# Optimization experiments

Measured on AMD Instinct MI355X. Metric: run time of the kernel, lower is better.

The kernel has to match this reference:

```python
import jax, jax.numpy as jnp
import numpy as np

B, N, M, D, H, K, V = 2, 2048, 2048, 1024, 16, 64, 64
MAX_WAVELENGTH = 10000
SCALE_FACTOR = 1.0


def rope(x, positions, max_wavelength, scale_factor):
    # x: [b, s, h, k]; positions: [b, s] int
    head_dim = x.shape[-1]
    fraction = 2.0 * jnp.arange(head_dim // 2, dtype=x.dtype) / head_dim
    timescale = jnp.asarray(max_wavelength, x.dtype) ** fraction            # [k/2]
    # scaled positions -> phase per (b, s, 1 head bcast, k/2)
    phase = (positions.astype(x.dtype) / scale_factor)[:, :, None, None] / timescale  # [b,s,1,k/2]
    sin, cos = jnp.sin(phase), jnp.cos(phase)
    x1, x2 = jnp.split(x, 2, axis=-1)
    return jnp.concatenate([x1 * cos - x2 * sin, x2 * cos + x1 * sin], axis=-1)


def setup_inputs() -> dict:
    key = jax.random.key(0)
    ks = jax.random.split(key, 8)
    scale = 1.0 / np.sqrt(D)  # keep logits numerically sane with random params
    inp = {
        "query": jax.random.normal(ks[0], (B, N, D), jnp.float32),
        "q_positions": jnp.broadcast_to(jnp.arange(N, dtype=jnp.int32), (B, N)),
        "key": jax.random.normal(ks[1], (B, M, D), jnp.float32),
        "k_positions": jnp.broadcast_to(jnp.arange(M, dtype=jnp.int32), (B, M)),
        "value": jax.random.normal(ks[2], (B, M, D), jnp.float32),
        "mask": jnp.ones((1, 1, N, M), dtype=bool),
        "P_q": jax.random.normal(ks[3], (H, D, K), jnp.float32) * scale,
        "P_k": jax.random.normal(ks[4], (H, D, K), jnp.float32) * scale,
        "P_v": jax.random.normal(ks[5], (H, D, V), jnp.float32) * scale,
        "P_o": jax.random.normal(ks[6], (H, D, V), jnp.float32) * scale,
    }
    return inp


def reference(query, q_positions, key, k_positions, value, mask, P_q, P_k, P_v, P_o):
    q = jnp.einsum('bnd,hdk->bnhk', query, P_q)
    k = jnp.einsum('bmd,hdk->bmhk', key, P_k)
    v = jnp.einsum('bmd,hdv->bmhv', value, P_v)
    q = rope(q, q_positions, MAX_WAVELENGTH, SCALE_FACTOR)
    k = rope(k, k_positions, MAX_WAVELENGTH, SCALE_FACTOR)
    logits = jnp.einsum('bnhk,bmhk->bhnm', q, k)
    if mask is not None:
        logits = jnp.where(mask, logits, -jnp.inf)
    weights = jax.nn.softmax(logits, axis=-1)
    o = jnp.einsum('bhnm,bmhv->bnhv', weights, v)
    return jnp.einsum('bnhv,hdv->bnd', o, P_o)
```

## Files before the change

kernel.cpp:

```cpp
#include <hip/hip_runtime.h>
#include <hip/hip_bf16.h>
#include <math.h>

#define B_ 2
#define N_ 2048
#define M_ 2048
#define D_ 1024
#define H_ 16


typedef _Float16 f16;
typedef f16  f16x2 __attribute__((ext_vector_type(2)));
typedef f16  f16x4 __attribute__((ext_vector_type(4)));
typedef f16  f16x8 __attribute__((ext_vector_type(8)));
typedef float f32x4  __attribute__((ext_vector_type(4)));
typedef float f32x16 __attribute__((ext_vector_type(16)));

#define MFMA16(a, b, c) __builtin_amdgcn_mfma_f32_16x16x32_f16((a), (b), (c), 0, 0, 0)
#define MFMA32(a, b, c) __builtin_amdgcn_mfma_f32_32x32x16_f16((a), (b), (c), 0, 0, 0)
#define LDST 72
#define EXP2(x) __builtin_amdgcn_exp2f(x)

static __device__ __forceinline__ unsigned int pk2(float a, float b) {
  auto h = __builtin_amdgcn_cvt_pkrtz(a, b);
  return __builtin_bit_cast(unsigned int, h);
}
static __device__ __forceinline__ float max3f(float a, float b, float c) {
  return fmaxf(fmaxf(a, b), c);
}

__global__ __launch_bounds__(256) void prep_all(
    const float* __restrict__ Pq, const float* __restrict__ Pk,
    const float* __restrict__ Pv, const float* __restrict__ Po,
    const int* __restrict__ qpos, const int* __restrict__ kpos,
    f16* __restrict__ Ptq, f16* __restrict__ Ptk, f16* __restrict__ Ptv,
    f16* __restrict__ Wo, float2* __restrict__ tabq, float2* __restrict__ tabk)
{
  __shared__ float Ts[64][65];
  const int z = blockIdx.y, x = blockIdx.x, tid = threadIdx.x;
  if (z < 3) {
    if (x >= 256) return;
    const float* P = (z == 0) ? Pq : (z == 1) ? Pk : Pv;
    f16* Pt = (z == 0) ? Ptq : (z == 1) ? Ptk : Ptv;
    const int d0 = (x & 15) * 64, h = x >> 4;
    #pragma unroll
    for (int it = 0; it < 4; ++it) {
      int fi = tid + 256 * it;
      int dr = fi >> 4, c4 = (fi & 15) << 2;
      float4 v = *(const float4*)(P + ((size_t)h * D_ + d0 + dr) * 64 + c4);
      Ts[dr][c4+0] = v.x; Ts[dr][c4+1] = v.y; Ts[dr][c4+2] = v.z; Ts[dr][c4+3] = v.w;
    }
    __syncthreads();
    const int c = tid >> 2, dp = (tid & 3) * 16;
    f16x8 w0, w1;
    #pragma unroll
    for (int i = 0; i < 8; ++i) { w0[i] = (f16)Ts[dp + i][c]; w1[i] = (f16)Ts[dp + 8 + i][c]; }
    f16* dst = Pt + ((size_t)h * 64 + c) * D_ + d0 + dp;
    *(f16x8*)dst = w0;
    *(f16x8*)(dst + 8) = w1;
  } else if (z == 3) {
    int e = (x * 256 + tid) * 4;
    if (e >= H_ * D_ * 64) return;
    int h = e >> 16, d = (e >> 6) & 1023, v = e & 63;
    float4 xx = *(const float4*)(Po + e);
    f16x4 w = {(f16)xx.x, (f16)xx.y, (f16)xx.z, (f16)xx.w};
    *(f16x4*)&Wo[(size_t)d * 1024 + h * 64 + v] = w;
  } else {
    if (x >= 512) return;
    int idx = x * 256 + tid;
    int r = idx >> 5, c = idx & 31;
    const int* pos = (z == 4) ? qpos : kpos;
    float2* tab = (z == 4) ? tabq : tabk;
    float fpos = (float)pos[r];
    float inv_ts = exp2f(-(float)c * 0.4152410118609203f);
    float ph = fpos * inv_ts, sn, cs;
    sincosf(ph, &sn, &cs);
    tab[idx] = make_float2(cs, sn);
  }
}

__global__ __launch_bounds__(256) void gemm_fused(
    const float* __restrict__ Aq, const float* __restrict__ Ak,
    const float* __restrict__ Av,
    const f16* __restrict__ Bq, const f16* __restrict__ Bk,
    const f16* __restrict__ Bv,
    const float2* __restrict__ tabq, const float2* __restrict__ tabk,
    f16* __restrict__ dq, f16* __restrict__ dk, f16* __restrict__ dv)
{
  __shared__ f16 As[128 * LDST];
  __shared__ f16 Bs[128 * LDST];
  const int tid = threadIdx.x, lane = tid & 63, wave = tid >> 6;
  const int quad = lane >> 4, l16 = lane & 15;
  const int lb = blockIdx.x + 8 * (int)blockIdx.y;
  const int xcd = lb & 7, t = lb >> 3;
  const int col0 = (t & 7) * 128;
  const int row0 = (xcd * 4 + (t >> 3)) * 128;
  const int op = blockIdx.z;
  const int wr = (wave >> 1) * 64, wc = (wave & 1) * 64;

  const float* A  = (op == 0) ? Aq : (op == 1) ? Ak : Av;
  const f16*  Bt  = (op == 0) ? Bq : (op == 1) ? Bk : Bv;

  f32x4 acc[4][4] = {};
  float4 apre[8];
  f16x8  bpre[4];

  #pragma unroll
  for (int it = 0; it < 8; ++it) {
    int fi = tid + 256 * it;
    int row = fi >> 4, c4 = (fi & 15) << 2;
    apre[it] = *(const float4*)(A + (size_t)(row0 + row) * 1024 + c4);
  }
  #pragma unroll
  for (int it = 0; it < 4; ++it) {
    int fi = tid + 256 * it;
    int row = fi >> 3, c8 = (fi & 7) * 8;
    bpre[it] = *(const f16x8*)(Bt + (size_t)(col0 + row) * 1024 + c8);
  }

  for (int k0 = 0; k0 < 1024; k0 += 64) {
    __syncthreads();
    #pragma unroll
    for (int it = 0; it < 8; ++it) {
      int fi = tid + 256 * it;
      int row = fi >> 4, c4 = (fi & 15) << 2;
      f16x4 hv = {(f16)apre[it].x, (f16)apre[it].y, (f16)apre[it].z, (f16)apre[it].w};
      *(f16x4*)&As[row * LDST + c4] = hv;
    }
    #pragma unroll
    for (int it = 0; it < 4; ++it) {
      int fi = tid + 256 * it;
      int row = fi >> 3, c8 = (fi & 7) * 8;
      *(f16x8*)&Bs[row * LDST + c8] = bpre[it];
    }
    __syncthreads();
    if (k0 + 64 < 1024) {
      #pragma unroll
      for (int it = 0; it < 8; ++it) {
        int fi = tid + 256 * it;
        int row = fi >> 4, c4 = (fi & 15) << 2;
        apre[it] = *(const float4*)(A + (size_t)(row0 + row) * 1024 + k0 + 64 + c4);
      }
      #pragma unroll
      for (int it = 0; it < 4; ++it) {
        int fi = tid + 256 * it;
        int row = fi >> 3, c8 = (fi & 7) * 8;
        bpre[it] = *(const f16x8*)(Bt + (size_t)(col0 + row) * 1024 + k0 + 64 + c8);
      }
    }
    #pragma unroll
    for (int ks = 0; ks < 2; ++ks) {
      f16x8 af[4], bf[4];
      #pragma unroll
      for (int i = 0; i < 4; ++i)
        af[i] = *(const f16x8*)&As[(wr + i * 16 + l16) * LDST + ks * 32 + quad * 8];
      #pragma unroll
      for (int j = 0; j < 4; ++j)
        bf[j] = *(const f16x8*)&Bs[(wc + j * 16 + l16) * LDST + ks * 32 + quad * 8];
      #pragma unroll
      for (int i = 0; i < 4; ++i)
        #pragma unroll
        for (int j = 0; j < 4; ++j)
          acc[i][j] = MFMA16(af[i], bf[j], acc[i][j]);
    }
  }

  if (op == 2) {
    #pragma unroll
    for (int i = 0; i < 4; ++i) {
      int r = row0 + wr + i * 16 + quad * 4;
      int b = r >> 11, s = r & 2047;
      #pragma unroll
      for (int j = 0; j < 4; ++j) {
        int col = col0 + wc + j * 16 + l16;
        int h = col >> 6, v = col & 63;
        f16x4 w = {(f16)acc[i][j][0], (f16)acc[i][j][1],
                   (f16)acc[i][j][2], (f16)acc[i][j][3]};
        *(f16x4*)&dv[((size_t)(b * H_ + h) * 64 + v) * 2048 + s] = w;
      }
    }
  } else {
    const float2* tab = (op == 0) ? tabq : tabk;
    f16* oq = (op == 0) ? dq : dk;
    #pragma unroll
    for (int i = 0; i < 4; ++i) {
      #pragma unroll
      for (int reg = 0; reg < 4; ++reg) {
        int r = row0 + wr + i * 16 + quad * 4 + reg;
        int b = r >> 11, s = r & 2047;
        #pragma unroll
        for (int j = 0; j < 2; ++j) {
          int col = col0 + wc + j * 16 + l16;
          int h = col >> 6, c = col & 63;
          float2 cs = tab[r * 32 + c];
          float x1 = acc[i][j][reg], x2 = acc[i][j + 2][reg];
          size_t base = ((size_t)(b * H_ + h) * 2048 + s) * 64;
          oq[base + c]      = (f16)(x1 * cs.x - x2 * cs.y);
          oq[base + c + 32] = (f16)(x2 * cs.x + x1 * cs.y);
        }
      }
    }
  }
}

__global__ __launch_bounds__(512, 4) void flash7b(
    const f16* __restrict__ q, const f16* __restrict__ k,
    const f16* __restrict__ vt, f16* __restrict__ o)
{
  __shared__ __align__(16) char smem[4 * 64 * LDST * sizeof(f16)];

  const int tid = threadIdx.x, lane = tid & 63, wave = tid >> 6;
  const int g = wave >> 2, w4 = wave & 3;
  const int L = lane >> 5, nl = lane & 31;
  const int lin = blockIdx.x + 16 * (blockIdx.y + 16 * (int)blockIdx.z);
  const int xcd = lin & 7, t = lin >> 3;
  const int hb = xcd * 4 + (t >> 4);
  const int n0 = (t & 15) * 128;
  const int h = hb & 15, b = hb >> 4;

  f16* Ks  = (f16*)smem + (size_t)g * (64 * LDST);
  f16* Vts = (f16*)smem + (size_t)(2 + g) * (64 * LDST);

  const f16* qb = q  + (size_t)(b * H_ + h) * N_ * 64;
  const f16* kb = k  + (size_t)(b * H_ + h) * M_ * 64 + (size_t)g * 1024 * 64;
  const f16* vb = vt + (size_t)(b * H_ + h) * 64 * M_ + g * 1024;

  f16x8 qf[4];
  #pragma unroll
  for (int gg = 0; gg < 4; ++gg)
    qf[gg] = *(const f16x8*)(qb + (size_t)(n0 + w4 * 32 + nl) * 64 + gg * 16 + L * 8);

  f32x16 acc[2] = {};
  float mst = -INFINITY;
  float lst = 0.f;
  const float L2E = 1.4426950408889634f;

  const int gtid = tid & 255;
  const int srow = gtid >> 2, soff = (gtid & 3) * 16;

  f16x8 kp0 = *(const f16x8*)(kb + (size_t)srow * 64 + soff);
  f16x8 kp1 = *(const f16x8*)(kb + (size_t)srow * 64 + soff + 8);
  f16x8 vp0 = *(const f16x8*)(vb + (size_t)srow * M_ + soff);
  f16x8 vp1 = *(const f16x8*)(vb + (size_t)srow * M_ + soff + 8);

  for (int m0 = 0; m0 < 1024; m0 += 64) {
    __syncthreads();
    *(f16x8*)&Ks[srow * LDST + soff]      = kp0;
    *(f16x8*)&Ks[srow * LDST + soff + 8]  = kp1;
    *(f16x8*)&Vts[srow * LDST + soff]     = vp0;
    *(f16x8*)&Vts[srow * LDST + soff + 8] = vp1;
    __syncthreads();
    if (m0 + 64 < 1024) {
      kp0 = *(const f16x8*)(kb + (size_t)(m0 + 64 + srow) * 64 + soff);
      kp1 = *(const f16x8*)(kb + (size_t)(m0 + 64 + srow) * 64 + soff + 8);
      vp0 = *(const f16x8*)(vb + (size_t)srow * M_ + m0 + 64 + soff);
      vp1 = *(const f16x8*)(vb + (size_t)srow * M_ + m0 + 64 + soff + 8);
    }

    f32x16 s[2] = {};
    __builtin_amdgcn_s_setprio(1);
    #pragma unroll
    for (int u = 0; u < 2; ++u)
      #pragma unroll
      for (int gg = 0; gg < 4; ++gg) {
        f16x8 af = *(const f16x8*)&Ks[(u * 32 + nl) * LDST + gg * 16 + L * 8];
        s[u] = MFMA32(af, qf[gg], s[u]);
      }
    __builtin_amdgcn_s_setprio(0);

    float a11[11];
    #pragma unroll
    for (int i = 0; i < 10; ++i) {
      int j = 3 * i;
      float x0 = (j < 16) ? s[0][j] : s[1][j - 16];
      float x1 = (j + 1 < 16) ? s[0][j + 1] : s[1][j - 15];
      float x2 = (j + 2 < 16) ? s[0][j + 2] : s[1][j - 14];
      a11[i] = max3f(x0, x1, x2);
    }
    a11[10] = fmaxf(s[1][14], s[1][15]);
    float b4_0 = max3f(a11[0], a11[1], a11[2]);
    float b4_1 = max3f(a11[3], a11[4], a11[5]);
    float b4_2 = max3f(a11[6], a11[7], a11[8]);
    float b4_3 = fmaxf(a11[9], a11[10]);
    float mx = fmaxf(fmaxf(b4_0, b4_1), fmaxf(b4_2, b4_3));
    mx = fmaxf(mx, __shfl_xor(mx, 32));
    float mx2 = mx * L2E;
    float m_new = fmaxf(mst, mx2);

    if (!__all(mx2 - mst <= 8.0f)) {
      float alpha = EXP2(mst - m_new);
      #pragma unroll
      for (int u = 0; u < 2; ++u)
        #pragma unroll
        for (int r = 0; r < 16; ++r) acc[u][r] *= alpha;
      lst *= alpha;
      mst = m_new;
    }

    #pragma unroll
    for (int u = 0; u < 2; ++u)
      #pragma unroll
      for (int r = 0; r < 16; ++r)
        s[u][r] = EXP2(s[u][r] * L2E - mst);

    unsigned int qw[2][4][2];
    #pragma unroll
    for (int u = 0; u < 2; ++u)
      #pragma unroll
      for (int rq = 0; rq < 4; ++rq) {
        qw[u][rq][0] = pk2(s[u][rq * 4 + 0], s[u][rq * 4 + 1]);
        qw[u][rq][1] = pk2(s[u][rq * 4 + 2], s[u][rq * 4 + 3]);
      }

#if __has_builtin(__builtin_amdgcn_fdot2)
    {
      const f16x2 one2 = {(f16)1.0f, (f16)1.0f};
      float sum = 0.f;
      #pragma unroll
      for (int u = 0; u < 2; ++u)
        #pragma unroll
        for (int rq = 0; rq < 4; ++rq)
          #pragma unroll
          for (int w = 0; w < 2; ++w)
            sum = __builtin_amdgcn_fdot2(
                __builtin_bit_cast(f16x2, qw[u][rq][w]), one2, sum, false);
      sum += __shfl_xor(sum, 32);
      lst += sum;
    }
#else
    {
      float ts[16];
      #pragma unroll
      for (int r = 0; r < 16; ++r) ts[r] = s[0][r] + s[1][r];
      #pragma unroll
      for (int st = 8; st >= 1; st >>= 1)
        #pragma unroll
        for (int r = 0; r < st; ++r) ts[r] += ts[r + st];
      float sum = ts[0];
      sum += __shfl_xor(sum, 32);
      lst += sum;
    }
#endif

    union PBu { unsigned int w[4]; f16x8 v; } pb[4];
    #pragma unroll
    for (int u = 0; u < 2; ++u)
      #pragma unroll
      for (int gg = 0; gg < 2; ++gg)
        #pragma unroll
        for (int w = 0; w < 2; ++w) {
          unsigned int a = qw[u][2 * gg][w], bb = qw[u][2 * gg + 1][w];
          asm volatile("v_permlane32_swap_b32 %0, %1" : "+v"(a), "+v"(bb));
          pb[2 * u + gg].w[w]     = a;
          pb[2 * u + gg].w[2 + w] = bb;
        }

    __builtin_amdgcn_s_setprio(1);
    #pragma unroll
    for (int u = 0; u < 2; ++u)
      #pragma unroll
      for (int gg = 0; gg < 4; ++gg) {
        f16x8 vf = *(const f16x8*)&Vts[(u * 32 + nl) * LDST + gg * 16 + L * 8];
        acc[u] = MFMA32(vf, pb[gg].v, acc[u]);
      }
    __builtin_amdgcn_s_setprio(0);
  }

  float* mrg = (float*)smem;
  const int mb = (w4 * 64 + lane) * 34;
  __syncthreads();
  if (g == 1) {
    #pragma unroll
    for (int r = 0; r < 16; ++r) { mrg[mb + r] = acc[0][r]; mrg[mb + 16 + r] = acc[1][r]; }
    mrg[mb + 32] = mst;
    mrg[mb + 33] = lst;
  }
  __syncthreads();
  if (g == 0) {
    float m1 = mrg[mb + 32], l1 = mrg[mb + 33];
    float Mm = fmaxf(mst, m1);
    float a0 = EXP2(mst - Mm), a1 = EXP2(m1 - Mm);
    float invl = 1.0f / (a0 * lst + a1 * l1);
    f16* ob = o + ((size_t)(b * N_ + n0 + w4 * 32 + nl) * 1024) + h * 64;
    #pragma unroll
    for (int u = 0; u < 2; ++u)
      #pragma unroll
      for (int rq = 0; rq < 4; ++rq) {
        f16x4 w;
        #pragma unroll
        for (int j = 0; j < 4; ++j)
          w[j] = (f16)((a0 * acc[u][rq * 4 + j] + a1 * mrg[mb + u * 16 + rq * 4 + j]) * invl);
        *(f16x4*)&ob[u * 32 + 8 * rq + 4 * L] = w;
      }
  }
}

__global__ __launch_bounds__(256) void gemm_out(
    const f16* __restrict__ A, const f16* __restrict__ Bt,
    float* __restrict__ out)
{
  __shared__ f16 As[128 * LDST];
  __shared__ f16 Bs[64 * LDST];
  const int tid = threadIdx.x, lane = tid & 63, wave = tid >> 6;
  const int quad = lane >> 4, l16 = lane & 15;
  const int lb = blockIdx.x + 16 * (int)blockIdx.y;
  const int xcd = lb & 7, t = lb >> 3;
  const int col0 = (t & 15) * 64;
  const int row0 = (xcd * 4 + (t >> 4)) * 128;
  const int wr = (wave >> 1) * 64, wc = (wave & 1) * 32;

  f32x4 acc[4][2] = {};
  f16x8 apre[4], bpre[2];

  #pragma unroll
  for (int it = 0; it < 4; ++it) {
    int fi = tid + 256 * it;
    int row = fi >> 3, c8 = (fi & 7) * 8;
    apre[it] = *(const f16x8*)(A + (size_t)(row0 + row) * 1024 + c8);
  }
  #pragma unroll
  for (int it = 0; it < 2; ++it) {
    int fi = tid + 256 * it;
    int row = fi >> 3, c8 = (fi & 7) * 8;
    bpre[it] = *(const f16x8*)(Bt + (size_t)(col0 + row) * 1024 + c8);
  }

  for (int k0 = 0; k0 < 1024; k0 += 64) {
    __syncthreads();
    #pragma unroll
    for (int it = 0; it < 4; ++it) {
      int fi = tid + 256 * it;
      int row = fi >> 3, c8 = (fi & 7) * 8;
      *(f16x8*)&As[row * LDST + c8] = apre[it];
    }
    #pragma unroll
    for (int it = 0; it < 2; ++it) {
      int fi = tid + 256 * it;
      int row = fi >> 3, c8 = (fi & 7) * 8;
      *(f16x8*)&Bs[row * LDST + c8] = bpre[it];
    }
    __syncthreads();
    if (k0 + 64 < 1024) {
      #pragma unroll
      for (int it = 0; it < 4; ++it) {
        int fi = tid + 256 * it;
        int row = fi >> 3, c8 = (fi & 7) * 8;
        apre[it] = *(const f16x8*)(A + (size_t)(row0 + row) * 1024 + k0 + 64 + c8);
      }
      #pragma unroll
      for (int it = 0; it < 2; ++it) {
        int fi = tid + 256 * it;
        int row = fi >> 3, c8 = (fi & 7) * 8;
        bpre[it] = *(const f16x8*)(Bt + (size_t)(col0 + row) * 1024 + k0 + 64 + c8);
      }
    }
    #pragma unroll
    for (int ks = 0; ks < 2; ++ks) {
      f16x8 af[4], bf[2];
      #pragma unroll
      for (int i = 0; i < 4; ++i)
        af[i] = *(const f16x8*)&As[(wr + i * 16 + l16) * LDST + ks * 32 + quad * 8];
      #pragma unroll
      for (int j = 0; j < 2; ++j)
        bf[j] = *(const f16x8*)&Bs[(wc + j * 16 + l16) * LDST + ks * 32 + quad * 8];
      #pragma unroll
      for (int i = 0; i < 4; ++i)
        #pragma unroll
        for (int j = 0; j < 2; ++j)
          acc[i][j] = MFMA16(af[i], bf[j], acc[i][j]);
    }
  }

  #pragma unroll
  for (int i = 0; i < 4; ++i)
    #pragma unroll
    for (int j = 0; j < 2; ++j)
      #pragma unroll
      for (int reg = 0; reg < 4; ++reg)
        out[(size_t)(row0 + wr + i * 16 + quad * 4 + reg) * 1024 +
            col0 + wc + j * 16 + l16] = acc[i][j][reg];
}

extern "C" void kernel_launch(void* const* d_in, const int* in_sizes, int n_in,
                              void* d_out, int out_size, void* d_ws, size_t ws_size,
                              hipStream_t stream) {
  (void)in_sizes; (void)n_in; (void)out_size; (void)ws_size;
  const float* query = (const float*)d_in[0];
  const int*   qpos  = (const int*)d_in[1];
  const float* key   = (const float*)d_in[2];
  const int*   kpos  = (const int*)d_in[3];
  const float* value = (const float*)d_in[4];
  const float* Pq = (const float*)d_in[6];
  const float* Pk = (const float*)d_in[7];
  const float* Pv = (const float*)d_in[8];
  const float* Po = (const float*)d_in[9];
  float* out = (float*)d_out;

  const size_t pm = (size_t)1024 * 1024;
  const size_t em = (size_t)B_ * H_ * 2048 * 64;
  f16* Ptq = (f16*)d_ws;
  f16* Ptk = Ptq + pm;
  f16* Ptv = Ptk + pm;
  f16* Wo  = Ptv + pm;
  f16* q_ws  = Wo + pm;
  f16* k_ws  = q_ws + em;
  f16* vt_ws = k_ws + em;
  f16* o_ws  = vt_ws + em;
  float2* tabq = (float2*)(o_ws + em);
  float2* tabk = tabq + (size_t)4096 * 32;

  dim3 blk(256);
  prep_all<<<dim3(1024, 6), blk, 0, stream>>>(
      Pq, Pk, Pv, Po, qpos, kpos, Ptq, Ptk, Ptv, Wo, tabq, tabk);

  gemm_fused<<<dim3(8, 32, 3), blk, 0, stream>>>(
      query, key, value, Ptq, Ptk, Ptv, tabq, tabk, q_ws, k_ws, vt_ws);

  flash7b<<<dim3(N_ / 128, H_, B_), dim3(512), 0, stream>>>(q_ws, k_ws, vt_ws, o_ws);

  gemm_out<<<dim3(16, 32), blk, 0, stream>>>(o_ws, Wo, out);
}
```

Before: 232.9 us.

## Pre-convert activations to fp16 and stage GEMM tiles via direct global-to-LDS loads

Adds a conversion pass in the prep kernel that casts query/key/value from fp32 to fp16 in workspace, so the projection GEMM reads half-width activations. Both the projection GEMM and the output GEMM now fill shared memory with global_load_lds (16-byte direct-to-LDS) instead of register prefetch plus ds_write. The padded LDS stride is dropped to fit the direct-load layout. In exchange, the register-level double-buffer overlap is gone, the extra conversion pass costs a full fp32 read plus fp16 write of the activations, and the unpadded layout may cause LDS bank conflicts on fragment reads.

```diff
diff --git a/kernel.cpp b/kernel.cpp
--- a/kernel.cpp
+++ b/kernel.cpp
@@ -21,6 +21,11 @@
 #define LDST 72
 #define EXP2(x) __builtin_amdgcn_exp2f(x)
 
+#define GLOAD_LDS(g, l)                                             \
+  __builtin_amdgcn_global_load_lds(                                 \
+      (const __attribute__((address_space(1))) void*)(g),           \
+      (__attribute__((address_space(3))) void*)(l), 16, 0, 0)
+
 static __device__ __forceinline__ unsigned int pk2(float a, float b) {
   auto h = __builtin_amdgcn_cvt_pkrtz(a, b);
   return __builtin_bit_cast(unsigned int, h);
@@ -33,8 +38,11 @@
     const float* __restrict__ Pq, const float* __restrict__ Pk,
     const float* __restrict__ Pv, const float* __restrict__ Po,
     const int* __restrict__ qpos, const int* __restrict__ kpos,
+    const float* __restrict__ Aq, const float* __restrict__ Ak,
+    const float* __restrict__ Av,
     f16* __restrict__ Ptq, f16* __restrict__ Ptk, f16* __restrict__ Ptv,
-    f16* __restrict__ Wo, float2* __restrict__ tabq, float2* __restrict__ tabk)
+    f16* __restrict__ Wo, float2* __restrict__ tabq, float2* __restrict__ tabk,
+    f16* __restrict__ A16q, f16* __restrict__ A16k, f16* __restrict__ A16v)
 {
   __shared__ float Ts[64][65];
   const int z = blockIdx.y, x = blockIdx.x, tid = threadIdx.x;
@@ -65,7 +73,7 @@
     float4 xx = *(const float4*)(Po + e);
     f16x4 w = {(f16)xx.x, (f16)xx.y, (f16)xx.z, (f16)xx.w};
     *(f16x4*)&Wo[(size_t)d * 1024 + h * 64 + v] = w;
-  } else {
+  } else if (z < 6) {
     if (x >= 512) return;
     int idx = x * 256 + tid;
     int r = idx >> 5, c = idx & 31;
@@ -76,19 +84,31 @@
     float ph = fpos * inv_ts, sn, cs;
     sincosf(ph, &sn, &cs);
     tab[idx] = make_float2(cs, sn);
+  } else {
+    const float* s = (z == 6) ? Aq : (z == 7) ? Ak : Av;
+    f16* d = (z == 6) ? A16q : (z == 7) ? A16k : A16v;
+    size_t e = ((size_t)x * 256 + tid) * 16;
+    #pragma unroll
+    for (int half = 0; half < 2; ++half) {
+      float4 v0 = *(const float4*)(s + e + half * 8);
+      float4 v1 = *(const float4*)(s + e + half * 8 + 4);
+      f16x8 w = {(f16)v0.x, (f16)v0.y, (f16)v0.z, (f16)v0.w,
+                 (f16)v1.x, (f16)v1.y, (f16)v1.z, (f16)v1.w};
+      *(f16x8*)(d + e + half * 8) = w;
+    }
   }
 }
 
 __global__ __launch_bounds__(256) void gemm_fused(
-    const float* __restrict__ Aq, const float* __restrict__ Ak,
-    const float* __restrict__ Av,
+    const f16* __restrict__ Aq, const f16* __restrict__ Ak,
+    const f16* __restrict__ Av,
     const f16* __restrict__ Bq, const f16* __restrict__ Bk,
     const f16* __restrict__ Bv,
     const float2* __restrict__ tabq, const float2* __restrict__ tabk,
     f16* __restrict__ dq, f16* __restrict__ dk, f16* __restrict__ dv)
 {
-  __shared__ f16 As[128 * LDST];
-  __shared__ f16 Bs[128 * LDST];
+  __shared__ f16 As[128 * 64];
+  __shared__ f16 Bs[128 * 64];
   const int tid = threadIdx.x, lane = tid & 63, wave = tid >> 6;
   const int quad = lane >> 4, l16 = lane & 15;
   const int lb = blockIdx.x + 8 * (int)blockIdx.y;
@@ -98,65 +118,32 @@
   const int op = blockIdx.z;
   const int wr = (wave >> 1) * 64, wc = (wave & 1) * 64;
 
-  const float* A  = (op == 0) ? Aq : (op == 1) ? Ak : Av;
-  const f16*  Bt  = (op == 0) ? Bq : (op == 1) ? Bk : Bv;
+  const f16* A  = (op == 0) ? Aq : (op == 1) ? Ak : Av;
+  const f16* Bt = (op == 0) ? Bq : (op == 1) ? Bk : Bv;
 
   f32x4 acc[4][4] = {};
-  float4 apre[8];
-  f16x8  bpre[4];
-
-  #pragma unroll
-  for (int it = 0; it < 8; ++it) {
-    int fi = tid + 256 * it;
-    int row = fi >> 4, c4 = (fi & 15) << 2;
-    apre[it] = *(const float4*)(A + (size_t)(row0 + row) * 1024 + c4);
-  }
-  #pragma unroll
-  for (int it = 0; it < 4; ++it) {
-    int fi = tid + 256 * it;
-    int row = fi >> 3, c8 = (fi & 7) * 8;
-    bpre[it] = *(const f16x8*)(Bt + (size_t)(col0 + row) * 1024 + c8);
-  }
+  const int srow = wave * 8 + (lane >> 3);
+  const int scol = (lane & 7) * 8;
 
   for (int k0 = 0; k0 < 1024; k0 += 64) {
     __syncthreads();
     #pragma unroll
-    for (int it = 0; it < 8; ++it) {
-      int fi = tid + 256 * it;
-      int row = fi >> 4, c4 = (fi & 15) << 2;
-      f16x4 hv = {(f16)apre[it].x, (f16)apre[it].y, (f16)apre[it].z, (f16)apre[it].w};
-      *(f16x4*)&As[row * LDST + c4] = hv;
-    }
-    #pragma unroll
-    for (int it = 0; it < 4; ++it) {
-      int fi = tid + 256 * it;
-      int row = fi >> 3, c8 = (fi & 7) * 8;
-      *(f16x8*)&Bs[row * LDST + c8] = bpre[it];
-    }
-    __syncthreads();
-    if (k0 + 64 < 1024) {
-      #pragma unroll
-      for (int it = 0; it < 8; ++it) {
-        int fi = tid + 256 * it;
-        int row = fi >> 4, c4 = (fi & 15) << 2;
-        apre[it] = *(const float4*)(A + (size_t)(row0 + row) * 1024 + k0 + 64 + c4);
-      }
-      #pragma unroll
-      for (int it = 0; it < 4; ++it) {
-        int fi = tid + 256 * it;
-        int row = fi >> 3, c8 = (fi & 7) * 8;
-        bpre[it] = *(const f16x8*)(Bt + (size_t)(col0 + row) * 1024 + k0 + 64 + c8);
-      }
-    }
+    for (int c = 0; c < 4; ++c) {
+      GLOAD_LDS(A  + (size_t)(row0 + c * 32 + srow) * 1024 + k0 + scol,
+                &As[c * 2048 + wave * 512 + lane * 8]);
+      GLOAD_LDS(Bt + (size_t)(col0 + c * 32 + srow) * 1024 + k0 + scol,
+                &Bs[c * 2048 + wave * 512 + lane * 8]);
+    }
+    __syncthreads();
     #pragma unroll
     for (int ks = 0; ks < 2; ++ks) {
       f16x8 af[4], bf[4];
       #pragma unroll
       for (int i = 0; i < 4; ++i)
-        af[i] = *(const f16x8*)&As[(wr + i * 16 + l16) * LDST + ks * 32 + quad * 8];
+        af[i] = *(const f16x8*)&As[(wr + i * 16 + l16) * 64 + ks * 32 + quad * 8];
       #pragma unroll
       for (int j = 0; j < 4; ++j)
-        bf[j] = *(const f16x8*)&Bs[(wc + j * 16 + l16) * LDST + ks * 32 + quad * 8];
+        bf[j] = *(const f16x8*)&Bs[(wc + j * 16 + l16) * 64 + ks * 32 + quad * 8];
       #pragma unroll
       for (int i = 0; i < 4; ++i)
         #pragma unroll
@@ -399,8 +386,8 @@
     const f16* __restrict__ A, const f16* __restrict__ Bt,
     float* __restrict__ out)
 {
-  __shared__ f16 As[128 * LDST];
-  __shared__ f16 Bs[64 * LDST];
+  __shared__ f16 As[128 * 64];
+  __shared__ f16 Bs[64 * 64];
   const int tid = threadIdx.x, lane = tid & 63, wave = tid >> 6;
   const int quad = lane >> 4, l16 = lane & 15;
   const int lb = blockIdx.x + 16 * (int)blockIdx.y;
@@ -410,59 +397,29 @@
   const int wr = (wave >> 1) * 64, wc = (wave & 1) * 32;
 
   f32x4 acc[4][2] = {};
-  f16x8 apre[4], bpre[2];
-
-  #pragma unroll
-  for (int it = 0; it < 4; ++it) {
-    int fi = tid + 256 * it;
-    int row = fi >> 3, c8 = (fi & 7) * 8;
-    apre[it] = *(const f16x8*)(A + (size_t)(row0 + row) * 1024 + c8);
-  }
-  #pragma unroll
-  for (int it = 0; it < 2; ++it) {
-    int fi = tid + 256 * it;
-    int row = fi >> 3, c8 = (fi & 7) * 8;
-    bpre[it] = *(const f16x8*)(Bt + (size_t)(col0 + row) * 1024 + c8);
-  }
+  const int srow = wave * 8 + (lane >> 3);
+  const int scol = (lane & 7) * 8;
 
   for (int k0 = 0; k0 < 1024; k0 += 64) {
     __syncthreads();
     #pragma unroll
-    for (int it = 0; it < 4; ++it) {
-      int fi = tid + 256 * it;
-      int row = fi >> 3, c8 = (fi & 7) * 8;
-      *(f16x8*)&As[row * LDST + c8] = apre[it];
-    }
-    #pragma unroll
-    for (int it = 0; it < 2; ++it) {
-      int fi = tid + 256 * it;
-      int row = fi >> 3, c8 = (fi & 7) * 8;
-      *(f16x8*)&Bs[row * LDST + c8] = bpre[it];
-    }
-    __syncthreads();
-    if (k0 + 64 < 1024) {
-      #pragma unroll
-      for (int it = 0; it < 4; ++it) {
-        int fi = tid + 256 * it;
-        int row = fi >> 3, c8 = (fi & 7) * 8;
-        apre[it] = *(const f16x8*)(A + (size_t)(row0 + row) * 1024 + k0 + 64 + c8);
-      }
-      #pragma unroll
-      for (int it = 0; it < 2; ++it) {
-        int fi = tid + 256 * it;
-        int row = fi >> 3, c8 = (fi & 7) * 8;
-        bpre[it] = *(const f16x8*)(Bt + (size_t)(col0 + row) * 1024 + k0 + 64 + c8);
-      }
-    }
+    for (int c = 0; c < 4; ++c)
+      GLOAD_LDS(A + (size_t)(row0 + c * 32 + srow) * 1024 + k0 + scol,
+                &As[c * 2048 + wave * 512 + lane * 8]);
+    #pragma unroll
+    for (int c = 0; c < 2; ++c)
+      GLOAD_LDS(Bt + (size_t)(col0 + c * 32 + srow) * 1024 + k0 + scol,
+                &Bs[c * 2048 + wave * 512 + lane * 8]);
+    __syncthreads();
     #pragma unroll
     for (int ks = 0; ks < 2; ++ks) {
       f16x8 af[4], bf[2];
       #pragma unroll
       for (int i = 0; i < 4; ++i)
-        af[i] = *(const f16x8*)&As[(wr + i * 16 + l16) * LDST + ks * 32 + quad * 8];
+        af[i] = *(const f16x8*)&As[(wr + i * 16 + l16) * 64 + ks * 32 + quad * 8];
       #pragma unroll
       for (int j = 0; j < 2; ++j)
-        bf[j] = *(const f16x8*)&Bs[(wc + j * 16 + l16) * LDST + ks * 32 + quad * 8];
+        bf[j] = *(const f16x8*)&Bs[(wc + j * 16 + l16) * 64 + ks * 32 + quad * 8];
       #pragma unroll
       for (int i = 0; i < 4; ++i)
         #pragma unroll
@@ -508,13 +465,17 @@
   f16* o_ws  = vt_ws + em;
   float2* tabq = (float2*)(o_ws + em);
   float2* tabk = tabq + (size_t)4096 * 32;
+  f16* a16q = (f16*)(tabk + (size_t)4096 * 32);
+  f16* a16k = a16q + em;
+  f16* a16v = a16k + em;
 
   dim3 blk(256);
-  prep_all<<<dim3(1024, 6), blk, 0, stream>>>(
-      Pq, Pk, Pv, Po, qpos, kpos, Ptq, Ptk, Ptv, Wo, tabq, tabk);
+  prep_all<<<dim3(1024, 9), blk, 0, stream>>>(
+      Pq, Pk, Pv, Po, qpos, kpos, query, key, value,
+      Ptq, Ptk, Ptv, Wo, tabq, tabk, a16q, a16k, a16v);
 
   gemm_fused<<<dim3(8, 32, 3), blk, 0, stream>>>(
-      query, key, value, Ptq, Ptk, Ptv, tabq, tabk, q_ws, k_ws, vt_ws);
+      a16q, a16k, a16v, Ptq, Ptk, Ptv, tabq, tabk, q_ws, k_ws, vt_ws);
 
   flash7b<<<dim3(N_ / 128, H_, B_), dim3(512), 0, stream>>>(q_ws, k_ws, vt_ws, o_ws);
 
```

Measured after the change: 241.5 us. 1.04x slower.
